# Performance work log

Hardware: AMD Instinct MI355X
Metric: run time of the kernel (lower is better)

The kernel has to match this reference:

```python
import jax, jax.numpy as jnp
import numpy as np

K = 7            # neighbor volumes (NNN heads)
PS = 10          # patch size
ADJ = PS // 2    # patch anchor offset (use_adj)
WOFF = 29 // 2   # search window half-size (ws=29)
KSEARCH = 224    # hardcoded in forward
T, C, E, HH, WW = 1, 8, 8, 64, 64


def _box1(a, axis):
    # sliding-window sum of length PS anchored at i-ADJ, zero outside
    pw = [(0, 0)] * a.ndim
    pw[axis] = (ADJ, PS - 1 - ADJ)
    ap = jnp.pad(a, pw)
    c = jnp.cumsum(ap, axis=axis)
    zp = [(0, 0)] * a.ndim
    zp[axis] = (1, 0)
    c = jnp.pad(c, zp)
    n = a.shape[axis]
    return jax.lax.slice_in_dim(c, PS, PS + n, axis=axis) - jax.lax.slice_in_dim(c, 0, n, axis=axis)


def box_sum(a):
    return _box1(_box1(a, -2), -1)


def setup_inputs():
    key = jax.random.key(0)
    ks = jax.random.split(key, 5)
    x = jax.random.normal(ks[0], (T, C, HH, WW), jnp.float32)
    xe = jax.random.normal(ks[1], (T, E, HH, WW), jnp.float32)
    ye = jax.random.normal(ks[2], (T, E, HH, WW), jnp.float32)
    y = jax.random.normal(ks[3], (T, C, HH, WW), jnp.float32)
    log_temp = 0.1 * jax.random.normal(ks[4], (T, 1, HH, WW), jnp.float32)
    return {"x": x, "xe": xe, "ye": ye, "y": y, "log_temp": log_temp}


def reference(x, xe, ye, y, log_temp):
    pad = lambda a: jnp.pad(a, ((0, 0), (0, 0), (1, 1), (1, 1)))
    x, xe, ye, y, log_temp = pad(x), pad(xe), pad(ye), pad(y), pad(log_temp)
    H, W = x.shape[-2:]
    Q = H * W
    xe0, ye0 = xe[0], ye[0]
    # search window offsets (ws x ws)
    dy, dx = np.meshgrid(np.arange(-WOFF, WOFF + 1), np.arange(-WOFF, WOFF + 1), indexing='ij')
    dy = jnp.asarray(dy.ravel()); dx = jnp.asarray(dx.ravel())
    nW = dy.shape[0]  # 841
    # patch squared norms (zero padded patches)
    n2_q = box_sum((ye0 ** 2).sum(0))   # (H,W)
    n2_db = box_sum((xe0 ** 2).sum(0))  # (H,W)
    xep = jnp.pad(xe0, ((0, 0), (WOFF, WOFF), (WOFF, WOFF)))
    n2p = jnp.pad(n2_db, WOFF)
    def shifted(d):
        s = jax.lax.dynamic_slice(xep, (0, WOFF + d[0], WOFF + d[1]), (E, H, W))
        n = jax.lax.dynamic_slice(n2p, (WOFF + d[0], WOFF + d[1]), (H, W))
        return s, n
    xe_s, n2_s = jax.vmap(shifted)(jnp.stack([dy, dx], -1))  # (nW,E,H,W),(nW,H,W)
    cross = box_sum((ye0[None] * xe_s).sum(1))               # (nW,H,W)
    dist = n2_q[None] + n2_s - 2.0 * cross                   # L2^2, (nW,H,W)
    qy = jnp.arange(H)[:, None]; qx = jnp.arange(W)[None, :]
    valid = ((qy[None] + dy[:, None, None] >= 0) & (qy[None] + dy[:, None, None] < H)
             & (qx[None] + dx[:, None, None] >= 0) & (qx[None] + dx[:, None, None] < W))
    self_m = (dy == 0) & (dx == 0)  # remove_self
    dist = jnp.where(valid & ~self_m[:, None, None], dist, 1e10)
    dist = dist.transpose(1, 2, 0).reshape(Q, nW)
    negd, idx = jax.lax.top_k(-dist, KSEARCH)  # closest KSEARCH, negd = -L2
    # avg-pooled log temperature per query patch
    lt = (box_sum(log_temp[0, 0]) / (PS * PS)).reshape(Q)
    # NeuralNearestNeighbors: iterative continuous top-k relaxation
    logits = negd / jnp.exp(lt)[:, None]
    Ws = []
    for _ in range(K):
        w = jax.nn.softmax(logits, axis=-1)
        logits = logits + jnp.log(jnp.clip(1.0 - w, 1e-6, None))
        Ws.append(w)
    Wk = jnp.stack(Ws)  # (K,Q,KSEARCH)
    # absolute candidate coords
    qyf = jnp.repeat(jnp.arange(H), W); qxf = jnp.tile(jnp.arange(W), H)
    ny = qyf[:, None] + dy[idx]; nx = qxf[:, None] + dx[idx]  # (Q,KSEARCH)
    # weighted patch sum (gather per patch offset)
    xpad = jnp.pad(x[0], ((0, 0), (ADJ, PS - 1 - ADJ), (ADJ, PS - 1 - ADJ)))
    z = jnp.zeros((K, Q, C, PS, PS), x.dtype)
    for oy in range(PS):
        for ox in range(PS):
            vals = xpad[:, ny + oy, nx + ox]  # (C,Q,KSEARCH)
            z = z.at[:, :, :, oy, ox].set(jnp.einsum('kqj,cqj->kqc', Wk, vals))
    # fold with counting (iFoldz): overlap-add of patches + coverage counts
    zp = z.transpose(1, 0, 2, 3, 4).reshape(H, W, K * C, PS, PS)
    buf = jnp.zeros((K * C, H + PS - 1, W + PS - 1), x.dtype)
    cnt = jnp.zeros((H + PS - 1, W + PS - 1), x.dtype)
    for oy in range(PS):
        for ox in range(PS):
            buf = buf.at[:, oy:oy + H, ox:ox + W].add(zp[:, :, :, oy, ox].transpose(2, 0, 1))
            cnt = cnt.at[oy:oy + H, ox:ox + W].add(1.0)
    vid = buf[:, ADJ:ADJ + H, ADJ:ADJ + W]
    zvid = cnt[ADJ:ADJ + H, ADJ:ADJ + W]
    zagg = vid / zvid[None]
    zagg = zagg.reshape(T, K, C, H, W) - y.reshape(T, 1, C, H, W)
    zagg = zagg.reshape(T, K * C, H, W)
    out = jnp.concatenate([y, zagg], axis=1)[..., 1:-1, 1:-1]
    return out
```

## Files before the change

### kernel.cpp

```cpp
#include <hip/hip_runtime.h>
#include <hip/hip_bf16.h>

#define HP    66
#define QTOT  (HP*HP)
#define LSTR  67
#define NWIN  29
#define NW    (NWIN*NWIN)
#define KK    7
#define WOFF2 14
#define NZ    15
#define QB    8
#define QBN   545
#define NIT   27
#define NSEG3 198


__global__ __launch_bounds__(256) void k_prep1(const float* __restrict__ x,
    const float* __restrict__ xe, const float* __restrict__ ye,
    const float* __restrict__ lt, float* __restrict__ ws) {
  int p = blockIdx.x * 256 + threadIdx.x;
  if (p >= QTOT) return;
  int i = p / HP, j = p % HP;
  bool in = (i >= 1 && i < HP-1 && j >= 1 && j < HP-1);
  int src = (i-1)*64 + (j-1);
  float vy[8], vx[8], vv[8];
  float sy = 0.f, sx = 0.f;
#pragma unroll
  for (int e = 0; e < 8; ++e) {
    vy[e] = in ? ye[e*4096 + src] : 0.f;
    vx[e] = in ? xe[e*4096 + src] : 0.f;
    vv[e] = in ? x [e*4096 + src] : 0.f;
    sy += vy[e]*vy[e]; sx += vx[e]*vx[e];
  }
  float4* yp = (float4*)(ws + (size_t)p*8);
  float4* xp = (float4*)(ws + 8*QTOT + (size_t)p*8);
  float4* vp = (float4*)(ws + 16*QTOT + (size_t)p*8);
  yp[0] = make_float4(vy[0], vy[1], vy[2], vy[3]);
  yp[1] = make_float4(vy[4], vy[5], vy[6], vy[7]);
  xp[0] = make_float4(vx[0], vx[1], vx[2], vx[3]);
  xp[1] = make_float4(vx[4], vx[5], vx[6], vx[7]);
  vp[0] = make_float4(vv[0], vv[1], vv[2], vv[3]);
  vp[1] = make_float4(vv[4], vv[5], vv[6], vv[7]);
  ws[24*QTOT + p] = sy;
  ws[25*QTOT + p] = sx;
  ws[26*QTOT + p] = in ? lt[src] : 0.f;
}

__global__ __launch_bounds__(256) void k_prep2(float* __restrict__ ws) {
  int p = blockIdx.x * 256 + threadIdx.x;
  if (p >= QTOT) return;
  int i = p / HP, j = p % HP;
  const float* sqye = ws + 24*QTOT;
  const float* sqxe = ws + 25*QTOT;
  const float* lt66 = ws + 26*QTOT;
  float a = 0.f, b = 0.f, c = 0.f;
  for (int u = -5; u <= 4; ++u) {
    int ii = i + u; if (ii < 0 || ii >= HP) continue;
    for (int v = -5; v <= 4; ++v) {
      int jj = j + v; if (jj < 0 || jj >= HP) continue;
      int o = ii*HP + jj;
      a += sqye[o]; b += sqxe[o]; c += lt66[o];
    }
  }
  ws[27*QTOT + p] = a;
  ws[28*QTOT + p] = b;
  ws[29*QTOT + p] = c * 0.01f;
}

__global__ __launch_bounds__(256) void k_dist(const float* __restrict__ ws,
                                              float* __restrict__ dist) {
  __shared__ float s[HP*LSTR];
  __shared__ float h[HP*LSTR];
  int w = blockIdx.x, tid = threadIdx.x;
  int dy = w / NWIN - WOFF2, dx = w % NWIN - WOFF2;
  const float* yex = ws;
  const float* xex = ws + 8*QTOT;
  const float* n2q  = ws + 27*QTOT;
  const float* n2db = ws + 28*QTOT;
  for (int p = tid; p < QTOT; p += 256) {
    int i = p / HP, j = p % HP;
    int ii = i + dy, jj = j + dx;
    float sv = 0.f;
    if (ii >= 0 && ii < HP && jj >= 0 && jj < HP) {
      int p2 = ii*HP + jj;
      const float4* yp = (const float4*)(yex + (size_t)p*8);
      const float4* xp = (const float4*)(xex + (size_t)p2*8);
      float4 a0 = yp[0], a1 = yp[1], b0 = xp[0], b1 = xp[1];
      sv += a0.x*b0.x; sv += a0.y*b0.y; sv += a0.z*b0.z; sv += a0.w*b0.w;
      sv += a1.x*b1.x; sv += a1.y*b1.y; sv += a1.z*b1.z; sv += a1.w*b1.w;
    }
    s[i*LSTR + j] = sv;
  }
  __syncthreads();
  if (tid < NSEG3) {
    int row = tid % HP, seg = tid / HP, c0 = seg*22;
    const float* ar = s + row*LSTR;
    float* hr = h + row*LSTR;
    float w9[9]; float sum = 0.f;
#pragma unroll
    for (int t = 0; t < 9; ++t) {
      int jj = c0 - 5 + t;
      float v = (jj >= 0) ? ar[jj] : 0.f;
      w9[t] = v; sum += v;
    }
#pragma unroll
    for (int t = 0; t < 22; ++t) {
      int j = c0 + t, jn = j + 4;
      float nv = (jn < HP) ? ar[jn] : 0.f;
      sum += nv;
      hr[j] = sum;
      sum -= w9[t % 9];
      w9[t % 9] = nv;
    }
  }
  __syncthreads();
  if (tid < NSEG3) {
    int col = tid % HP, seg = tid / HP, r0 = seg*22;
    float w9[9]; float sum = 0.f;
#pragma unroll
    for (int t = 0; t < 9; ++t) {
      int ii = r0 - 5 + t;
      float v = (ii >= 0) ? h[ii*LSTR + col] : 0.f;
      w9[t] = v; sum += v;
    }
#pragma unroll
    for (int t = 0; t < 22; ++t) {
      int i = r0 + t, in2 = i + 4;
      float nv = (in2 < HP) ? h[in2*LSTR + col] : 0.f;
      sum += nv;
      float cr = sum;
      int p = i*HP + col;
      int ii = i + dy, jj = col + dx;
      bool valid = (ii >= 0 && ii < HP && jj >= 0 && jj < HP);
      float dv = 1e10f;
      if (valid && !(dy == 0 && dx == 0))
        dv = n2q[p] + n2db[ii*HP + jj] - 2.f * cr;
      dist[w*QTOT + p] = dv;
      sum -= w9[t % 9];
      w9[t % 9] = nv;
    }
  }
}

__global__ __launch_bounds__(256) void k_weights(const float* __restrict__ ws,
    const float* __restrict__ dist, __hip_bfloat16* __restrict__ wf) {
  __shared__ float mh[32], sh[32];
  int tid = threadIdx.x;
  int qq = tid & (QB-1);
  int qb = blockIdx.x;
  int q = qb * QB + qq;
  bool qok = q < QTOT;
  int qs = qok ? q : (QTOT - 1);
  int wg = tid >> 3;
  int wave = tid >> 6;
  float invT = __expf(-ws[29*QTOT + qs]);
  float lv[NIT];
#pragma unroll
  for (int it = 0; it < NIT; ++it) {
    int w = wg + it*32;
    lv[it] = (qok && w < NW) ? (-dist[w*QTOT + qs] * invT) : -3.0e38f;
  }
  for (int k = 0; k < KK; ++k) {
    float pm = -3.0e38f;
#pragma unroll
    for (int it = 0; it < NIT; ++it) pm = fmaxf(pm, lv[it]);
    pm = fmaxf(pm, __shfl_xor(pm, 8, 64));
    pm = fmaxf(pm, __shfl_xor(pm, 16, 64));
    pm = fmaxf(pm, __shfl_xor(pm, 32, 64));
    if ((tid & 63) < QB) mh[wave*QB + qq] = pm;
    __syncthreads();
    float m = fmaxf(fmaxf(mh[qq], mh[QB+qq]), fmaxf(mh[2*QB+qq], mh[3*QB+qq]));
    float psum = 0.f;
#pragma unroll
    for (int it = 0; it < NIT; ++it) psum += __expf(lv[it] - m);
    psum += __shfl_xor(psum, 8, 64);
    psum += __shfl_xor(psum, 16, 64);
    psum += __shfl_xor(psum, 32, 64);
    if ((tid & 63) < QB) sh[wave*QB + qq] = psum;
    __syncthreads();
    float invden = 1.0f / (sh[qq] + sh[QB+qq] + sh[2*QB+qq] + sh[3*QB+qq]);
    size_t bkq = ((size_t)k*QBN + qb)*NW;
#pragma unroll
    for (int it = 0; it < NIT; ++it) {
      int w = wg + it*32;
      if (qok && w < NW) {
        float wgt = __expf(lv[it] - m) * invden;
        wf[(bkq + w)*8 + qq] = __float2bfloat16(wgt);
        if (k < KK-1 && wgt > 1e-9f)
          lv[it] += __logf(fmaxf(1.f - wgt, 1e-6f));
      }
    }
    __syncthreads();
  }
}

__global__ __launch_bounds__(256) void k_boxw(__hip_bfloat16* __restrict__ wfp) {
  __shared__ uint4 au4[546];
  __shared__ uint4 hu4[546];
  int bid = blockIdx.x;
  int l = (bid & 7)*736 + (bid >> 3);
  if (l >= KK*NW) return;
  int k = l / NW, w = l % NW;
  uint4* u4 = (uint4*)wfp;
  size_t pb = ((size_t)k*QBN)*NW + w;
  int tid = threadIdx.x;
  for (int qb = tid; qb < QBN; qb += 256)
    au4[qb] = u4[pb + (size_t)qb*NW];
  if (tid < 12) ((unsigned short*)au4)[4356 + tid] = 0;
  __syncthreads();
  const unsigned short* a16 = (const unsigned short*)au4;
  unsigned short* h16 = (unsigned short*)hu4;
  for (int task = tid; task < 396; task += 256) {
    int row = task % HP, seg = task / HP, c0 = seg*11;
    const unsigned short* ar = a16 + row*HP;
    unsigned short* hr = h16 + row*HP;
    float w9[9]; float sum = 0.f;
#pragma unroll
    for (int t = 0; t < 9; ++t) {
      int jj = c0 - 4 + t;
      float v = (jj >= 0) ? __uint_as_float((unsigned)ar[jj] << 16) : 0.f;
      w9[t] = v; sum += v;
    }
#pragma unroll
    for (int t = 0; t < 11; ++t) {
      int j = c0 + t, jn = j + 5;
      float nv = (jn < HP) ? __uint_as_float((unsigned)ar[jn] << 16) : 0.f;
      sum += nv;
      hr[j] = __bfloat16_as_ushort(__float2bfloat16(sum));
      sum -= w9[t % 9];
      w9[t % 9] = nv;
    }
  }
  __syncthreads();
  unsigned short* a16w = (unsigned short*)au4;
  for (int task = tid; task < 396; task += 256) {
    int col = task % HP, seg = task / HP, r0 = seg*11;
    float w9[9]; float sum = 0.f;
#pragma unroll
    for (int t = 0; t < 9; ++t) {
      int ii = r0 - 4 + t;
      float v = (ii >= 0) ? __uint_as_float((unsigned)h16[ii*HP + col] << 16) : 0.f;
      w9[t] = v; sum += v;
    }
#pragma unroll
    for (int t = 0; t < 11; ++t) {
      int i = r0 + t, in2 = i + 5;
      float nv = (in2 < HP) ? __uint_as_float((unsigned)h16[in2*HP + col] << 16) : 0.f;
      sum += nv;
      a16w[i*HP + col] = __bfloat16_as_ushort(__float2bfloat16(sum));
      sum -= w9[t % 9];
      w9[t % 9] = nv;
    }
  }
  __syncthreads();
  for (int qb = tid; qb < QBN; qb += 256)
    u4[pb + (size_t)qb*NW] = au4[qb];
}

__global__ __launch_bounds__(256) void k_contract(const float* __restrict__ ws,
    const unsigned short* __restrict__ wfu, float* __restrict__ accb2) {
  __shared__ float xt[17][44][8];
  int t = blockIdx.x, z = blockIdx.y, k = blockIdx.z, tid = threadIdx.x;
  int I0 = (t >> 2) * 16, J0 = (t & 3) * 16;
  int dylo = -WOFF2 + 2*z;
  int gy0 = I0 + 1 + dylo, gx0 = J0 - 13;
  const float* x66i = ws + 16*QTOT;
  for (int idx = tid; idx < 17*44; idx += 256) {
    int r = idx / 44, cc = idx % 44;
    int gy = gy0 + r, gx = gx0 + cc;
    float4 v0 = make_float4(0.f,0.f,0.f,0.f), v1 = v0;
    if (gy >= 0 && gy < HP && gx >= 0 && gx < HP) {
      const float4* xp = (const float4*)(x66i + (size_t)(gy*HP + gx)*8);
      v0 = xp[0]; v1 = xp[1];
    }
    float4* d = (float4*)&xt[r][cc][0];
    d[0] = v0; d[1] = v1;
  }
  __syncthreads();
  int il = tid >> 4, jl = tid & 15;
  int I = I0 + 1 + il, J = J0 + 1 + jl;
  int pix = I*HP + J;
  int qb = pix >> 3, q7 = pix & 7;
  size_t cb = (((size_t)k*QBN + qb)*NW)*8 + q7;
  float acc[8];
#pragma unroll
  for (int c = 0; c < 8; ++c) acc[c] = 0.f;
  int ndd = (z == NZ-1) ? 1 : 2;
  for (int dd = 0; dd < ndd; ++dd) {
    int wrow = (dylo + dd + WOFF2) * NWIN;
    const unsigned short* wp = wfu + cb + (size_t)wrow*8;
    unsigned short wv[NWIN];
#pragma unroll
    for (int dxw = 0; dxw < NWIN; ++dxw) wv[dxw] = wp[dxw*8];
    int r = il + dd;
#pragma unroll
    for (int dxw = 0; dxw < NWIN; ++dxw) {
      float wgt = __uint_as_float((unsigned)wv[dxw] << 16);
      const float4* xr = (const float4*)&xt[r][jl + dxw][0];
      float4 x0 = xr[0], x1 = xr[1];
      acc[0] += wgt * x0.x; acc[1] += wgt * x0.y;
      acc[2] += wgt * x0.z; acc[3] += wgt * x0.w;
      acc[4] += wgt * x1.x; acc[5] += wgt * x1.y;
      acc[6] += wgt * x1.z; acc[7] += wgt * x1.w;
    }
  }
  int px64 = (I-1)*64 + (J-1);
#pragma unroll
  for (int c = 0; c < 8; ++c)
    accb2[((z*56 + k*8 + c)*4096) + px64] = acc[c];
}

__global__ __launch_bounds__(256) void k_final(const float* __restrict__ y,
    const float* __restrict__ accb2, float* __restrict__ out) {
  int idx = blockIdx.x * 256 + threadIdx.x;
  int ch = idx >> 12, px = idx & 4095;
  if (ch < 8) { out[idx] = y[ch*4096 + px]; return; }
  int kc = ch - 8, c = kc & 7;
  int i = px >> 6, j = px & 63;
  int I = i + 1, J = j + 1;
  int cy = min(I+5, HP-1) - max(I-4, 0) + 1;
  int cx = min(J+5, HP-1) - max(J-4, 0) + 1;
  float s = 0.f;
  for (int z = 0; z < NZ; ++z) s += accb2[(z*56 + kc)*4096 + px];
  out[idx] = s / (float)(cy*cx) - y[c*4096 + px];
}

extern "C" void kernel_launch(void* const* d_in, const int* in_sizes, int n_in,
                              void* d_out, int out_size, void* d_ws, size_t ws_size,
                              hipStream_t stream) {
  const float* x  = (const float*)d_in[0];
  const float* xe = (const float*)d_in[1];
  const float* ye = (const float*)d_in[2];
  const float* y  = (const float*)d_in[3];
  const float* lt = (const float*)d_in[4];
  float* ws   = (float*)d_ws;
  float* dist = ws + 30*QTOT;
  __hip_bfloat16* wf = (__hip_bfloat16*)(dist + (size_t)NW*QTOT);
  float* accb2 = dist;
  float* out = (float*)d_out;

  k_prep1<<<(QTOT + 255)/256, 256, 0, stream>>>(x, xe, ye, lt, ws);
  k_prep2<<<(QTOT + 255)/256, 256, 0, stream>>>(ws);
  k_dist<<<NW, 256, 0, stream>>>(ws, dist);
  k_weights<<<QBN, 256, 0, stream>>>(ws, dist, wf);
  k_boxw<<<KK*NW, 256, 0, stream>>>(wf);
  k_contract<<<dim3(16, NZ, KK), 256, 0, stream>>>(ws, (const unsigned short*)wf, accb2);
  k_final<<<out_size/256, 256, 0, stream>>>(y, accb2, out);
}
```

Baseline: 147.6 us.

## Stage dist output through LDS and write box-filtered weights pixel-contiguous

```diff
diff --git a/kernel.cpp b/kernel.cpp
--- a/kernel.cpp
+++ b/kernel.cpp
@@ -3,7 +3,6 @@
 
 #define HP    66
 #define QTOT  (HP*HP)
-#define LSTR  67
 #define NWIN  29
 #define NW    (NWIN*NWIN)
 #define KK    7
@@ -13,6 +12,7 @@
 #define QBN   545
 #define NIT   27
 #define NSEG3 198
+#define PSTR  4368
 
 
 __global__ __launch_bounds__(256) void k_prep1(const float* __restrict__ x,
@@ -69,8 +69,9 @@
 
 __global__ __launch_bounds__(256) void k_dist(const float* __restrict__ ws,
                                               float* __restrict__ dist) {
-  __shared__ float s[HP*LSTR];
-  __shared__ float h[HP*LSTR];
+  __shared__ float4 s4[QTOT/4];
+  __shared__ float h[QTOT];
+  float* s = (float*)s4;
   int w = blockIdx.x, tid = threadIdx.x;
   int dy = w / NWIN - WOFF2, dx = w % NWIN - WOFF2;
   const float* yex = ws;
@@ -89,13 +90,13 @@
       sv += a0.x*b0.x; sv += a0.y*b0.y; sv += a0.z*b0.z; sv += a0.w*b0.w;
       sv += a1.x*b1.x; sv += a1.y*b1.y; sv += a1.z*b1.z; sv += a1.w*b1.w;
     }
-    s[i*LSTR + j] = sv;
+    s[p] = sv;
   }
   __syncthreads();
   if (tid < NSEG3) {
     int row = tid % HP, seg = tid / HP, c0 = seg*22;
-    const float* ar = s + row*LSTR;
-    float* hr = h + row*LSTR;
+    const float* ar = s + row*HP;
+    float* hr = h + row*HP;
     float w9[9]; float sum = 0.f;
 #pragma unroll
     for (int t = 0; t < 9; ++t) {
@@ -120,13 +121,13 @@
 #pragma unroll
     for (int t = 0; t < 9; ++t) {
       int ii = r0 - 5 + t;
-      float v = (ii >= 0) ? h[ii*LSTR + col] : 0.f;
+      float v = (ii >= 0) ? h[ii*HP + col] : 0.f;
       w9[t] = v; sum += v;
     }
 #pragma unroll
     for (int t = 0; t < 22; ++t) {
       int i = r0 + t, in2 = i + 4;
-      float nv = (in2 < HP) ? h[in2*LSTR + col] : 0.f;
+      float nv = (in2 < HP) ? h[in2*HP + col] : 0.f;
       sum += nv;
       float cr = sum;
       int p = i*HP + col;
@@ -135,11 +136,15 @@
       float dv = 1e10f;
       if (valid && !(dy == 0 && dx == 0))
         dv = n2q[p] + n2db[ii*HP + jj] - 2.f * cr;
-      dist[w*QTOT + p] = dv;
+      s[p] = dv;
       sum -= w9[t % 9];
       w9[t % 9] = nv;
     }
   }
+  __syncthreads();
+  float4* dq = (float4*)(dist + (size_t)w*QTOT);
+  for (int p4 = tid; p4 < QTOT/4; p4 += 256)
+    dq[p4] = s4[p4];
 }
 
 __global__ __launch_bounds__(256) void k_weights(const float* __restrict__ ws,
@@ -194,14 +199,15 @@
   }
 }
 
-__global__ __launch_bounds__(256) void k_boxw(__hip_bfloat16* __restrict__ wfp) {
+__global__ __launch_bounds__(256) void k_boxw(const __hip_bfloat16* __restrict__ wfa,
+                                              __hip_bfloat16* __restrict__ wfb) {
   __shared__ uint4 au4[546];
   __shared__ uint4 hu4[546];
   int bid = blockIdx.x;
   int l = (bid & 7)*736 + (bid >> 3);
   if (l >= KK*NW) return;
   int k = l / NW, w = l % NW;
-  uint4* u4 = (uint4*)wfp;
+  const uint4* u4 = (const uint4*)wfa;
   size_t pb = ((size_t)k*QBN)*NW + w;
   int tid = threadIdx.x;
   for (int qb = tid; qb < QBN; qb += 256)
@@ -253,12 +259,13 @@
     }
   }
   __syncthreads();
-  for (int qb = tid; qb < QBN; qb += 256)
-    u4[pb + (size_t)qb*NW] = au4[qb];
+  uint4* out4 = (uint4*)(wfb + ((size_t)k*NW + w)*PSTR);
+  for (int qb = tid; qb < 546; qb += 256)
+    out4[qb] = au4[qb];
 }
 
 __global__ __launch_bounds__(256) void k_contract(const float* __restrict__ ws,
-    const unsigned short* __restrict__ wfu, float* __restrict__ accb2) {
+    const unsigned short* __restrict__ wfb, float* __restrict__ accb2) {
   __shared__ float xt[17][44][8];
   int t = blockIdx.x, z = blockIdx.y, k = blockIdx.z, tid = threadIdx.x;
   int I0 = (t >> 2) * 16, J0 = (t & 3) * 16;
@@ -280,18 +287,16 @@
   int il = tid >> 4, jl = tid & 15;
   int I = I0 + 1 + il, J = J0 + 1 + jl;
   int pix = I*HP + J;
-  int qb = pix >> 3, q7 = pix & 7;
-  size_t cb = (((size_t)k*QBN + qb)*NW)*8 + q7;
   float acc[8];
 #pragma unroll
   for (int c = 0; c < 8; ++c) acc[c] = 0.f;
   int ndd = (z == NZ-1) ? 1 : 2;
   for (int dd = 0; dd < ndd; ++dd) {
     int wrow = (dylo + dd + WOFF2) * NWIN;
-    const unsigned short* wp = wfu + cb + (size_t)wrow*8;
+    const unsigned short* wp = wfb + ((size_t)k*NW + wrow)*PSTR + pix;
     unsigned short wv[NWIN];
 #pragma unroll
-    for (int dxw = 0; dxw < NWIN; ++dxw) wv[dxw] = wp[dxw*8];
+    for (int dxw = 0; dxw < NWIN; ++dxw) wv[dxw] = wp[(size_t)dxw*PSTR];
     int r = il + dd;
 #pragma unroll
     for (int dxw = 0; dxw < NWIN; ++dxw) {
@@ -335,15 +340,16 @@
   const float* lt = (const float*)d_in[4];
   float* ws   = (float*)d_ws;
   float* dist = ws + 30*QTOT;
-  __hip_bfloat16* wf = (__hip_bfloat16*)(dist + (size_t)NW*QTOT);
+  __hip_bfloat16* wfa = (__hip_bfloat16*)(dist + (size_t)NW*QTOT);
+  __hip_bfloat16* wfb = wfa + (size_t)KK*QBN*NW*8;
   float* accb2 = dist;
   float* out = (float*)d_out;
 
   k_prep1<<<(QTOT + 255)/256, 256, 0, stream>>>(x, xe, ye, lt, ws);
   k_prep2<<<(QTOT + 255)/256, 256, 0, stream>>>(ws);
   k_dist<<<NW, 256, 0, stream>>>(ws, dist);
-  k_weights<<<QBN, 256, 0, stream>>>(ws, dist, wf);
-  k_boxw<<<KK*NW, 256, 0, stream>>>(wf);
-  k_contract<<<dim3(16, NZ, KK), 256, 0, stream>>>(ws, (const unsigned short*)wf, accb2);
+  k_weights<<<QBN, 256, 0, stream>>>(ws, dist, wfa);
+  k_boxw<<<KK*NW, 256, 0, stream>>>(wfa, wfb);
+  k_contract<<<dim3(16, NZ, KK), 256, 0, stream>>>(ws, (const unsigned short*)wfb, accb2);
   k_final<<<out_size/256, 256, 0, stream>>>(y, accb2, out);
 }
```

Result: no change. 145.3 us (-1.6%).
